# Performance work log

Measured on AMD Instinct MI355X. Metric: run time of the kernel, lower is better.

Reference implementation:

```python
import jax, jax.numpy as jnp
import numpy as np

NEG_SLOPE = 0.2  # PyG GATConv default


def _gat_layer(h_in, W, a_src, a_dst, b, src, dst, n_nodes, heads, out_dim):
    """One GATConv layer (PyG semantics: messages flow src -> dst,
    softmax over incoming edges of each dst node)."""
    h = (h_in @ W).reshape(n_nodes, heads, out_dim)          # [N,H,C]
    alpha_s = jnp.sum(h * a_src, axis=-1)                    # [N,H]
    alpha_d = jnp.sum(h * a_dst, axis=-1)                    # [N,H]
    e = jax.nn.leaky_relu(alpha_s[src] + alpha_d[dst], NEG_SLOPE)  # [E,H]
    # segment softmax over dst groups (numerically stable)
    m = jax.ops.segment_max(e, dst, num_segments=n_nodes)    # [N,H]
    ex = jnp.exp(e - m[dst])                                 # [E,H]
    s = jax.ops.segment_sum(ex, dst, num_segments=n_nodes)   # [N,H]
    alpha = ex / (s[dst] + 1e-16)                            # [E,H]
    msg = h[src] * alpha[:, :, None]                         # [E,H,C]
    out = jax.ops.segment_sum(msg, dst, num_segments=n_nodes)  # [N,H,C]
    return out.reshape(n_nodes, heads * out_dim) + b


def setup_inputs() -> dict:
    N, E = 50000, 800000
    IN, HID, H = 128, 64, 4
    key = jax.random.key(0)
    ks = jax.random.split(key, 10)
    x = jax.random.normal(ks[0], (N, IN), dtype=jnp.float32)
    edge_index = jax.random.randint(ks[1], (2, E), 0, N, dtype=jnp.int64)
    sc = 0.05
    return {
        "x": x,
        "edge_index": edge_index,
        "W1": jax.random.normal(ks[2], (IN, H * HID), dtype=jnp.float32) * sc,
        "att_src1": jax.random.normal(ks[3], (H, HID), dtype=jnp.float32) * sc,
        "att_dst1": jax.random.normal(ks[4], (H, HID), dtype=jnp.float32) * sc,
        "b1": jnp.zeros((H * HID,), dtype=jnp.float32),
        "W2": jax.random.normal(ks[5], (H * HID, HID), dtype=jnp.float32) * sc,
        "att_src2": jax.random.normal(ks[6], (1, HID), dtype=jnp.float32) * sc,
        "att_dst2": jax.random.normal(ks[7], (1, HID), dtype=jnp.float32) * sc,
        "b2": jnp.zeros((HID,), dtype=jnp.float32),
    }


def reference(x, edge_index, W1, att_src1, att_dst1, b1, W2, att_src2, att_dst2, b2):
    N = x.shape[0]
    H, HID = att_src1.shape
    # add self loops (PyG GATConv default add_self_loops=True)
    loops = jnp.arange(N, dtype=edge_index.dtype)
    src = jnp.concatenate([edge_index[0], loops])
    dst = jnp.concatenate([edge_index[1], loops])
    h = _gat_layer(x, W1, att_src1, att_dst1, b1, src, dst, N, H, HID)
    h = jax.nn.relu(h)
    out = _gat_layer(h, W2, att_src2, att_dst2, b2, src, dst, N, 1, HID)
    return out
```

## Files before the change

### kernel.cpp

```cpp
#include <hip/hip_runtime.h>
#include <cstdint>

#define LRELU_SLOPE 0.2f
#define ELL_K 48

typedef short bf16x8_t __attribute__((ext_vector_type(8)));
typedef float f32x4_t  __attribute__((ext_vector_type(4)));

__device__ __forceinline__ float bf2f(unsigned int u) { return __uint_as_float(u << 16); }
__device__ __forceinline__ unsigned short f2bf(float f) {
    unsigned int x = __float_as_uint(f);
    return (unsigned short)((x + 0x7fffu + ((x >> 16) & 1u)) >> 16);
}
__device__ __forceinline__ unsigned short f2h(float f) {
    union { unsigned short u; _Float16 h; } cv; cv.h = (_Float16)f; return cv.u;
}
__device__ __forceinline__ float h2f(unsigned short u) {
    union { unsigned short u; _Float16 h; } cv; cv.u = u; return (float)cv.h;
}

struct PrepDesc { const void* ssrc[6]; float* sdst[6]; int slen[6]; };
__global__ __launch_bounds__(256) void prep_k(const unsigned short* __restrict__ xh,
                                              const int* __restrict__ ei32,
                                              const void* __restrict__ w1raw,
                                              const void* __restrict__ w2raw,
                                              unsigned short* __restrict__ Wt1,
                                              unsigned short* __restrict__ Wt2,
                                              PrepDesc d, int* __restrict__ flags,
                                              int* __restrict__ deg, int N) {
    __shared__ int s_ei, s_cnt;
    if (threadIdx.x == 0) { s_ei = 0; s_cnt = 0; }
    __syncthreads();
    const int t = threadIdx.x;
    int e_or = 0;
#pragma unroll
    for (int j = 0; j < 4; j++) if (ei32[2 * (t * 4 + j) + 1] != 0) e_or = 1;
    if (e_or) atomicOr(&s_ei, 1);
    int c = 0;
#pragma unroll
    for (int j = 0; j < 8; j++) {
        unsigned short h = xh[t * 8 + j];
        int e = (h >> 7) & 0xFF;
        if (e >= 117 && e < 134) c++;
    }
    atomicAdd(&s_cnt, c);
    __syncthreads();
    const int isb = (s_cnt >= 1600) ? 1 : 0;
    if (blockIdx.x == 0 && t == 0) { flags[0] = s_ei; flags[1] = isb; }
    const int gstride = gridDim.x * blockDim.x;
    const int gid = blockIdx.x * blockDim.x + t;
    for (int i = gid; i < 128 * 256; i += gstride) {
        int k = i >> 8, n = i & 255;
        unsigned short b = isb ? ((const unsigned short*)w1raw)[i] : f2bf(((const float*)w1raw)[i]);
        Wt1[n * 128 + k] = b;
    }
    for (int i = gid; i < 256 * 64; i += gstride) {
        int k = i >> 6, n = i & 63;
        unsigned short b = isb ? ((const unsigned short*)w2raw)[i] : f2bf(((const float*)w2raw)[i]);
        Wt2[n * 256 + k] = b;
    }
#pragma unroll
    for (int s = 0; s < 6; s++)
        for (int i = gid; i < d.slen[s]; i += gstride) {
            float v = isb ? bf2f((unsigned int)((const unsigned short*)d.ssrc[s])[i])
                          : ((const float*)d.ssrc[s])[i];
            d.sdst[s][i] = v;
        }
    for (int i = gid; i < N; i += gstride) deg[i] = 0;
}

__global__ __launch_bounds__(256) void gemm1_k(const void* __restrict__ xraw,
                                               const unsigned short* __restrict__ Wt,
                                               const float* __restrict__ asw_,
                                               const float* __restrict__ adw_,
                                               unsigned short* __restrict__ h,
                                               float* __restrict__ as_, float* __restrict__ ad_,
                                               int M, const int* __restrict__ flags) {
    __shared__ unsigned short xs[64 * 136];
    const int tid = threadIdx.x;
    const long row0 = (long)blockIdx.x * 64;
    if (flags[1] != 0) {
        const uint4* xv = (const uint4*)xraw;
        const long base = row0 * 16;
        const long lim = (long)M * 16 - base;
#pragma unroll
        for (int i = 0; i < 4; i++) {
            int idx = tid + i * 256;
            uint4 v;
            if (idx < lim) v = xv[base + idx];
            else { v.x = v.y = v.z = v.w = 0u; }
            int r = idx >> 4, c8 = idx & 15;
            *(uint4*)&xs[r * 136 + c8 * 8] = v;
        }
    } else {
        const float4* xv = (const float4*)xraw;
        const long base = row0 * 32;
        const long lim = (long)M * 32 - base;
#pragma unroll
        for (int i = 0; i < 8; i++) {
            int idx = tid + i * 256;
            float4 v;
            if (idx < lim) v = xv[base + idx];
            else { v.x = v.y = v.z = v.w = 0.f; }
            int r = idx >> 5, c4 = idx & 31;
            ushort4 o;
            o.x = f2bf(v.x); o.y = f2bf(v.y); o.z = f2bf(v.z); o.w = f2bf(v.w);
            *(ushort4*)&xs[r * 136 + c4 * 4] = o;
        }
    }
    __syncthreads();
    const int wv = tid >> 6;
    const int lane = tid & 63;
    const int l16 = lane & 15, quad = lane >> 4;
    bf16x8_t af[4];
#pragma unroll
    for (int ks = 0; ks < 4; ks++)
        af[ks] = *(const bf16x8_t*)&xs[(wv * 16 + l16) * 136 + ks * 32 + quad * 8];
    float psA[4] = {0.f, 0.f, 0.f, 0.f}, pdA[4] = {0.f, 0.f, 0.f, 0.f};
#pragma unroll
    for (int t = 0; t < 16; t++) {
        f32x4_t acc = {0.f, 0.f, 0.f, 0.f};
#pragma unroll
        for (int ks = 0; ks < 4; ks++) {
            bf16x8_t bf = *(const bf16x8_t*)(Wt + (size_t)(t * 16 + l16) * 128 + ks * 32 + quad * 8);
            acc = __builtin_amdgcn_mfma_f32_16x16x32_bf16(af[ks], bf, acc, 0, 0, 0);
        }
        const float aswv = asw_[t * 16 + l16];
        const float adwv = adw_[t * 16 + l16];
#pragma unroll
        for (int r = 0; r < 4; r++) {
            long grow = row0 + wv * 16 + quad * 4 + r;
            if (grow < M) h[grow * 256 + t * 16 + l16] = f2bf(acc[r]);
            psA[r] = fmaf(acc[r], aswv, psA[r]);
            pdA[r] = fmaf(acc[r], adwv, pdA[r]);
        }
        if ((t & 3) == 3) {
            const int hd = t >> 2;
#pragma unroll
            for (int r = 0; r < 4; r++) {
                float ps = psA[r], pd = pdA[r];
#pragma unroll
                for (int o = 8; o > 0; o >>= 1) {
                    ps += __shfl_down(ps, o, 16);
                    pd += __shfl_down(pd, o, 16);
                }
                long grow = row0 + wv * 16 + quad * 4 + r;
                if (l16 == 0 && grow < M) { as_[grow * 4 + hd] = ps; ad_[grow * 4 + hd] = pd; }
                psA[r] = 0.f; pdA[r] = 0.f;
            }
        }
    }
}

__global__ void ell_k(const int* __restrict__ ei, int E, int N,
                      const int* __restrict__ flags, int* __restrict__ deg,
                      int* __restrict__ ell_src, uint2* __restrict__ ell_pw,
                      const float* __restrict__ as1, const float* __restrict__ ad1) {
    int i = blockIdx.x * blockDim.x + threadIdx.x;
    int T = E + N;
    if (i >= T) return;
    int is64 = (flags[0] == 0);
    int s, d;
    if (i < E) {
        s = is64 ? ei[2 * (long)i] : ei[i];
        long k = (long)E + i;
        d = is64 ? ei[2 * k] : ei[k];
    } else { s = d = i - E; }
    if ((unsigned)d >= (unsigned)N) return;
    if ((unsigned)s >= (unsigned)N) s = 0;
    int r = atomicAdd(&deg[d], 1);
    if (r >= ELL_K) return;
    long slot = (long)d * ELL_K + r;
    ell_src[slot] = s;
    float4 a = ((const float4*)as1)[s];
    float4 b = ((const float4*)ad1)[d];
    float e0 = a.x + b.x, e1 = a.y + b.y, e2 = a.z + b.z, e3 = a.w + b.w;
    e0 = e0 > 0.f ? e0 : LRELU_SLOPE * e0;
    e1 = e1 > 0.f ? e1 : LRELU_SLOPE * e1;
    e2 = e2 > 0.f ? e2 : LRELU_SLOPE * e2;
    e3 = e3 > 0.f ? e3 : LRELU_SLOPE * e3;
    uint2 p;
    p.x = (unsigned)f2h(__expf(e0)) | ((unsigned)f2h(__expf(e1)) << 16);
    p.y = (unsigned)f2h(__expf(e2)) | ((unsigned)f2h(__expf(e3)) << 16);
    ell_pw[slot] = p;
}

__global__ __launch_bounds__(256) void gemm2_k(const unsigned short* __restrict__ x,
                                               const unsigned short* __restrict__ Wt,
                                               const float* __restrict__ asw_,
                                               const float* __restrict__ adw_,
                                               unsigned short* __restrict__ h,
                                               float* __restrict__ as_, float* __restrict__ ad_,
                                               int M) {
    __shared__ unsigned short xs[64 * 264];
    const int tid = threadIdx.x;
    const long row0 = (long)blockIdx.x * 64;
    const uint4* xv = (const uint4*)x;
    const long base = row0 * 32;
    const long lim = (long)M * 32 - base;
#pragma unroll
    for (int i = 0; i < 8; i++) {
        int idx = tid + i * 256;
        uint4 v;
        if (idx < lim) v = xv[base + idx];
        else { v.x = v.y = v.z = v.w = 0u; }
        int r = idx >> 5, c8 = idx & 31;
        *(uint4*)&xs[r * 264 + c8 * 8] = v;
    }
    __syncthreads();
    const int wv = tid >> 6;
    const int lane = tid & 63;
    const int l16 = lane & 15, quad = lane >> 4;
    bf16x8_t af[8];
#pragma unroll
    for (int ks = 0; ks < 8; ks++)
        af[ks] = *(const bf16x8_t*)&xs[(wv * 16 + l16) * 264 + ks * 32 + quad * 8];
    float psA[4] = {0.f, 0.f, 0.f, 0.f}, pdA[4] = {0.f, 0.f, 0.f, 0.f};
#pragma unroll
    for (int t = 0; t < 4; t++) {
        f32x4_t acc = {0.f, 0.f, 0.f, 0.f};
#pragma unroll
        for (int ks = 0; ks < 8; ks++) {
            bf16x8_t bf = *(const bf16x8_t*)(Wt + (size_t)(t * 16 + l16) * 256 + ks * 32 + quad * 8);
            acc = __builtin_amdgcn_mfma_f32_16x16x32_bf16(af[ks], bf, acc, 0, 0, 0);
        }
        const float aswv = asw_[t * 16 + l16];
        const float adwv = adw_[t * 16 + l16];
#pragma unroll
        for (int r = 0; r < 4; r++) {
            long grow = row0 + wv * 16 + quad * 4 + r;
            if (grow < M) h[grow * 64 + t * 16 + l16] = f2bf(acc[r]);
            psA[r] = fmaf(acc[r], aswv, psA[r]);
            pdA[r] = fmaf(acc[r], adwv, pdA[r]);
        }
    }
#pragma unroll
    for (int r = 0; r < 4; r++) {
        float ps = psA[r], pd = pdA[r];
#pragma unroll
        for (int o = 8; o > 0; o >>= 1) { ps += __shfl_down(ps, o, 16); pd += __shfl_down(pd, o, 16); }
        long grow = row0 + wv * 16 + quad * 4 + r;
        if (l16 == 0 && grow < M) { as_[grow] = ps; ad_[grow] = pd; }
    }
}

#define B20(M) M(0) M(1) M(2) M(3) M(4) M(5) M(6) M(7) M(8) M(9) \
               M(10) M(11) M(12) M(13) M(14) M(15) M(16) M(17) M(18) M(19)

__global__ __launch_bounds__(256) void agg1_k(const uint4* __restrict__ hfeat,
                                              const int* __restrict__ deg,
                                              const int* __restrict__ ell_src,
                                              const uint2* __restrict__ ell_pw,
                                              const float* __restrict__ bias,
                                              unsigned short* __restrict__ outb, int N) {
    const int tid = threadIdx.x;
    const int g = tid >> 5;
    const int c = tid & 31;
    const long node = (long)blockIdx.x * 8 + g;
    if (node >= N) return;
    const int hh = c >> 3;
    const bool lo = hh < 2;
    const int sh = (hh & 1) << 4;
    const long beg = node * ELL_K;
    const int dv = deg[node];
    const int siA = ell_src[beg + c];
    const int siB = ell_src[beg + 32 + (c & 15)];
    const uint2 pAv = ell_pw[beg + c];
    const uint2 pBv = ell_pw[beg + 32 + (c & 15)];
    const unsigned pAx = pAv.x, pAy = pAv.y, pBx = pBv.x, pBy = pBv.y;
    const int cnt = dv < ELL_K ? dv : ELL_K;
    float a0 = 0.f, a1 = 0.f, a2 = 0.f, a3 = 0.f;
    float a4 = 0.f, a5 = 0.f, a6 = 0.f, a7 = 0.f, s = 0.f;
#define EDGE8(v, p) { \
        a0 = fmaf(p, __uint_as_float((v).x << 16), a0); \
        a1 = fmaf(p, __uint_as_float((v).x & 0xffff0000u), a1); \
        a2 = fmaf(p, __uint_as_float((v).y << 16), a2); \
        a3 = fmaf(p, __uint_as_float((v).y & 0xffff0000u), a3); \
        a4 = fmaf(p, __uint_as_float((v).z << 16), a4); \
        a5 = fmaf(p, __uint_as_float((v).z & 0xffff0000u), a5); \
        a6 = fmaf(p, __uint_as_float((v).w << 16), a6); \
        a7 = fmaf(p, __uint_as_float((v).w & 0xffff0000u), a7); \
        s += p; }
#define DECL1(k) uint4 vv##k;
#define ISSUE1(k) if (j + k < cnt) { \
        const int e = j + k; \
        const int sv = __shfl((e < 32) ? siA : siB, e & 31, 32); \
        vv##k = hfeat[(long)sv * 32 + c]; }
#define CONS1(k) if (j + k < cnt) { \
        const int e = j + k; \
        const unsigned bx = (unsigned)__shfl((int)((e < 32) ? pAx : pBx), e & 31, 32); \
        const unsigned by = (unsigned)__shfl((int)((e < 32) ? pAy : pBy), e & 31, 32); \
        const unsigned pwu = lo ? bx : by; \
        const float p = h2f((unsigned short)((pwu >> sh) & 0xffffu)); \
        EDGE8(vv##k, p) }
    {
        const int j = 0;
        B20(DECL1)
        B20(ISSUE1)
        B20(CONS1)
    }
    if (cnt > 20) {
        const int j = 20;
        B20(DECL1)
        B20(ISSUE1)
        B20(CONS1)
        if (cnt > 40) {
            const int j2 = 40;
#define ISSUE1b(k) if (j2 + k < cnt) { \
            const int e = j2 + k; \
            const int sv = __shfl((e < 32) ? siA : siB, e & 31, 32); \
            vv##k = hfeat[(long)sv * 32 + c]; }
#define CONS1b(k) if (j2 + k < cnt) { \
            const int e = j2 + k; \
            const unsigned bx = (unsigned)__shfl((int)((e < 32) ? pAx : pBx), e & 31, 32); \
            const unsigned by = (unsigned)__shfl((int)((e < 32) ? pAy : pBy), e & 31, 32); \
            const unsigned pwu = lo ? bx : by; \
            const float p = h2f((unsigned short)((pwu >> sh) & 0xffffu)); \
            EDGE8(vv##k, p) }
            ISSUE1b(0) ISSUE1b(1) ISSUE1b(2) ISSUE1b(3)
            ISSUE1b(4) ISSUE1b(5) ISSUE1b(6) ISSUE1b(7)
            CONS1b(0) CONS1b(1) CONS1b(2) CONS1b(3)
            CONS1b(4) CONS1b(5) CONS1b(6) CONS1b(7)
#undef ISSUE1b
#undef CONS1b
        }
    }
#undef DECL1
#undef ISSUE1
#undef CONS1
#undef EDGE8
    const float4 b0 = ((const float4*)bias)[2 * c];
    const float4 b1 = ((const float4*)bias)[2 * c + 1];
    const float inv = 1.f / s;
    uint4 o;
    o.x = (unsigned)f2bf(fmaxf(fmaf(a0, inv, b0.x), 0.f)) |
          ((unsigned)f2bf(fmaxf(fmaf(a1, inv, b0.y), 0.f)) << 16);
    o.y = (unsigned)f2bf(fmaxf(fmaf(a2, inv, b0.z), 0.f)) |
          ((unsigned)f2bf(fmaxf(fmaf(a3, inv, b0.w), 0.f)) << 16);
    o.z = (unsigned)f2bf(fmaxf(fmaf(a4, inv, b1.x), 0.f)) |
          ((unsigned)f2bf(fmaxf(fmaf(a5, inv, b1.y), 0.f)) << 16);
    o.w = (unsigned)f2bf(fmaxf(fmaf(a6, inv, b1.z), 0.f)) |
          ((unsigned)f2bf(fmaxf(fmaf(a7, inv, b1.w), 0.f)) << 16);
    ((uint4*)outb)[node * 32 + c] = o;
}

__global__ __launch_bounds__(256) void agg2_k(const unsigned short* __restrict__ hfeat,
                                              const float* __restrict__ as_,
                                              const float* __restrict__ ad_,
                                              const int* __restrict__ deg,
                                              const int* __restrict__ ell_src,
                                              const float* __restrict__ bias,
                                              unsigned short* __restrict__ outb,
                                              float* __restrict__ outf,
                                              const int* __restrict__ flags, int N) {
    const int tid = threadIdx.x;
    const int g = tid >> 4;
    const int c = tid & 15;
    const long node = (long)blockIdx.x * 16 + g;
    if (node >= N) return;
    const long beg = node * ELL_K;
    const int dv = deg[node];
    const int rA = ell_src[beg + c];
    const int rB = ell_src[beg + 16 + c];
    const int rC = ell_src[beg + 32 + c];
    const float adn = ad_[node];
    const int cnt = dv < ELL_K ? dv : ELL_K;
    const int sA = (c      < cnt) ? rA : 0;
    const int sB = (c + 16 < cnt) ? rB : 0;
    const int sC = (c + 32 < cnt) ? rC : 0;
    const float avA = as_[sA];
    const float avB = as_[sB];
    const float avC = as_[sC];
    const uint2* hv = (const uint2*)hfeat;
    float sm = 0.f, a0 = 0.f, a1 = 0.f, a2 = 0.f, a3 = 0.f;
#define EDGE4(v, p) { \
        a0 = fmaf(p, __uint_as_float((v).x << 16), a0); \
        a1 = fmaf(p, __uint_as_float((v).x & 0xffff0000u), a1); \
        a2 = fmaf(p, __uint_as_float((v).y << 16), a2); \
        a3 = fmaf(p, __uint_as_float((v).y & 0xffff0000u), a3); \
        sm += p; }
#define DECL2(k) uint2 vv##k;
#define ISSUE2(k) if (j + k < cnt) { \
        const int e = j + k; \
        const int sv = __shfl((e < 16) ? sA : ((e < 32) ? sB : sC), e & 15, 16); \
        vv##k = hv[(long)sv * 16 + c]; }
#define CONS2(k) if (j + k < cnt) { \
        const int e = j + k; \
        const float av = __shfl((e < 16) ? avA : ((e < 32) ? avB : avC), e & 15, 16); \
        float t = av + adn; t = t > 0.f ? t : LRELU_SLOPE * t; \
        const float p = __expf(t); \
        EDGE4(vv##k, p) }
    {
        const int j = 0;
        B20(DECL2)
        B20(ISSUE2)
        B20(CONS2)
    }
    if (cnt > 20) {
        const int j = 20;
        B20(DECL2)
        B20(ISSUE2)
        B20(CONS2)
        if (cnt > 40) {
            const int j2 = 40;
#define ISSUE2b(k) if (j2 + k < cnt) { \
            const int e = j2 + k; \
            const int sv = __shfl((e < 16) ? sA : ((e < 32) ? sB : sC), e & 15, 16); \
            vv##k = hv[(long)sv * 16 + c]; }
#define CONS2b(k) if (j2 + k < cnt) { \
            const int e = j2 + k; \
            const float av = __shfl((e < 16) ? avA : ((e < 32) ? avB : avC), e & 15, 16); \
            float t = av + adn; t = t > 0.f ? t : LRELU_SLOPE * t; \
            const float p = __expf(t); \
            EDGE4(vv##k, p) }
            ISSUE2b(0) ISSUE2b(1) ISSUE2b(2) ISSUE2b(3)
            ISSUE2b(4) ISSUE2b(5) ISSUE2b(6) ISSUE2b(7)
            CONS2b(0) CONS2b(1) CONS2b(2) CONS2b(3)
            CONS2b(4) CONS2b(5) CONS2b(6) CONS2b(7)
#undef ISSUE2b
#undef CONS2b
        }
    }
#undef DECL2
#undef ISSUE2
#undef CONS2
#undef EDGE4
    const float inv = 1.f / sm;
    const float4 bi = ((const float4*)bias)[c];
    const float v0 = fmaf(a0, inv, bi.x);
    const float v1 = fmaf(a1, inv, bi.y);
    const float v2 = fmaf(a2, inv, bi.z);
    const float v3 = fmaf(a3, inv, bi.w);
    if (flags[1] != 0) {
        uint2 o;
        o.x = (unsigned)f2bf(v0) | ((unsigned)f2bf(v1) << 16);
        o.y = (unsigned)f2bf(v2) | ((unsigned)f2bf(v3) << 16);
        ((uint2*)outb)[node * 16 + c] = o;
    } else {
        float4 o; o.x = v0; o.y = v1; o.z = v2; o.w = v3;
        ((float4*)outf)[node * 16 + c] = o;
    }
}

static inline size_t alignup(size_t v, size_t a) { return (v + a - 1) & ~(a - 1); }

extern "C" void kernel_launch(void* const* d_in, const int* in_sizes, int n_in,
                              void* d_out, int out_size, void* d_ws, size_t ws_size,
                              hipStream_t stream) {
    const void* x  = d_in[0];
    const int*  ei = (const int*)d_in[1];

    const int N = in_sizes[0] / 128;
    const int E = in_sizes[1] / 2;
    const int T = E + N;

    size_t off = 0;
    char* w = (char*)d_ws;
    auto take = [&](size_t bytes) { void* p = w + off; off = alignup(off + bytes, 256); return p; };

    int*   flags = (int*)take(256);
    unsigned short* Wt1 = (unsigned short*)take((size_t)256 * 128 * 2);
    unsigned short* Wt2 = (unsigned short*)take((size_t)64 * 256 * 2);
    float* as1w = (float*)take(256 * 4);
    float* ad1w = (float*)take(256 * 4);
    float* b1f  = (float*)take(256 * 4);
    float* as2w = (float*)take(64 * 4);
    float* ad2w = (float*)take(64 * 4);
    float* b2f  = (float*)take(64 * 4);
    unsigned short* h1b   = (unsigned short*)take((size_t)N * 256 * 2);
    unsigned short* act1b = (unsigned short*)take((size_t)N * 256 * 2);
    float* as1 = (float*)take((size_t)N * 4 * 4);
    float* ad1 = (float*)take((size_t)N * 4 * 4);
    float* as2 = (float*)take((size_t)N * 4);
    float* ad2 = (float*)take((size_t)N * 4);
    int* deg   = (int*)take((size_t)N * 4);
    int* ell_src = (int*)take((size_t)N * ELL_K * 4);
    uint2* ell_pw = (uint2*)take((size_t)N * ELL_K * 8);
    unsigned short* h2b = h1b;

    PrepDesc pd;
    pd.ssrc[0] = d_in[3]; pd.sdst[0] = as1w; pd.slen[0] = 256;
    pd.ssrc[1] = d_in[4]; pd.sdst[1] = ad1w; pd.slen[1] = 256;
    pd.ssrc[2] = d_in[5]; pd.sdst[2] = b1f;  pd.slen[2] = 256;
    pd.ssrc[3] = d_in[7]; pd.sdst[3] = as2w; pd.slen[3] = 64;
    pd.ssrc[4] = d_in[8]; pd.sdst[4] = ad2w; pd.slen[4] = 64;
    pd.ssrc[5] = d_in[9]; pd.sdst[5] = b2f;  pd.slen[5] = 64;
    prep_k<<<64, 256, 0, stream>>>((const unsigned short*)x, ei, d_in[2], d_in[6],
                                   Wt1, Wt2, pd, flags, deg, N);

    gemm1_k<<<(N + 63) / 64, 256, 0, stream>>>(x, Wt1, as1w, ad1w, h1b, as1, ad1, N, flags);
    ell_k<<<(T + 255) / 256, 256, 0, stream>>>(ei, E, N, flags, deg, ell_src, ell_pw, as1, ad1);
    agg1_k<<<(N + 7) / 8, 256, 0, stream>>>((const uint4*)h1b, deg, ell_src, ell_pw, b1f, act1b, N);
    gemm2_k<<<(N + 63) / 64, 256, 0, stream>>>(act1b, Wt2, as2w, ad2w, h2b, as2, ad2, N);
    agg2_k<<<(N + 15) / 16, 256, 0, stream>>>(h2b, as2, ad2, deg, ell_src, b2f,
                                              (unsigned short*)d_out, (float*)d_out, flags, N);
}
```

Baseline: 290.2 us.

## Fuse layer-2 GEMM into layer-1 aggregation kernel via LDS tile

The layer-1 aggregation now writes its 8 activated node rows into shared memory, and one wave then runs the layer-2 MFMA projection plus the attention dot products in the same block. This drops the separate gemm2 launch and the write and reread of the N×256 bf16 activation buffer. In exchange, each block pads its 16-row MFMA tile with 8 zero rows, so half the MFMA work is wasted. It also adds a __syncthreads and a serial GEMM tail on one wave while the other three sit idle, and every block rereads Wt2 from cache.

```diff
diff --git a/kernel.cpp b/kernel.cpp
--- a/kernel.cpp
+++ b/kernel.cpp
@@ -185,90 +185,45 @@
     ell_pw[slot] = p;
 }
 
-__global__ __launch_bounds__(256) void gemm2_k(const unsigned short* __restrict__ x,
-                                               const unsigned short* __restrict__ Wt,
-                                               const float* __restrict__ asw_,
-                                               const float* __restrict__ adw_,
-                                               unsigned short* __restrict__ h,
-                                               float* __restrict__ as_, float* __restrict__ ad_,
-                                               int M) {
-    __shared__ unsigned short xs[64 * 264];
-    const int tid = threadIdx.x;
-    const long row0 = (long)blockIdx.x * 64;
-    const uint4* xv = (const uint4*)x;
-    const long base = row0 * 32;
-    const long lim = (long)M * 32 - base;
-#pragma unroll
-    for (int i = 0; i < 8; i++) {
-        int idx = tid + i * 256;
-        uint4 v;
-        if (idx < lim) v = xv[base + idx];
-        else { v.x = v.y = v.z = v.w = 0u; }
-        int r = idx >> 5, c8 = idx & 31;
-        *(uint4*)&xs[r * 264 + c8 * 8] = v;
-    }
-    __syncthreads();
-    const int wv = tid >> 6;
-    const int lane = tid & 63;
-    const int l16 = lane & 15, quad = lane >> 4;
-    bf16x8_t af[8];
-#pragma unroll
-    for (int ks = 0; ks < 8; ks++)
-        af[ks] = *(const bf16x8_t*)&xs[(wv * 16 + l16) * 264 + ks * 32 + quad * 8];
-    float psA[4] = {0.f, 0.f, 0.f, 0.f}, pdA[4] = {0.f, 0.f, 0.f, 0.f};
-#pragma unroll
-    for (int t = 0; t < 4; t++) {
-        f32x4_t acc = {0.f, 0.f, 0.f, 0.f};
-#pragma unroll
-        for (int ks = 0; ks < 8; ks++) {
-            bf16x8_t bf = *(const bf16x8_t*)(Wt + (size_t)(t * 16 + l16) * 256 + ks * 32 + quad * 8);
-            acc = __builtin_amdgcn_mfma_f32_16x16x32_bf16(af[ks], bf, acc, 0, 0, 0);
-        }
-        const float aswv = asw_[t * 16 + l16];
-        const float adwv = adw_[t * 16 + l16];
-#pragma unroll
-        for (int r = 0; r < 4; r++) {
-            long grow = row0 + wv * 16 + quad * 4 + r;
-            if (grow < M) h[grow * 64 + t * 16 + l16] = f2bf(acc[r]);
-            psA[r] = fmaf(acc[r], aswv, psA[r]);
-            pdA[r] = fmaf(acc[r], adwv, pdA[r]);
-        }
-    }
-#pragma unroll
-    for (int r = 0; r < 4; r++) {
-        float ps = psA[r], pd = pdA[r];
-#pragma unroll
-        for (int o = 8; o > 0; o >>= 1) { ps += __shfl_down(ps, o, 16); pd += __shfl_down(pd, o, 16); }
-        long grow = row0 + wv * 16 + quad * 4 + r;
-        if (l16 == 0 && grow < M) { as_[grow] = ps; ad_[grow] = pd; }
-    }
-}
-
 #define B20(M) M(0) M(1) M(2) M(3) M(4) M(5) M(6) M(7) M(8) M(9) \
                M(10) M(11) M(12) M(13) M(14) M(15) M(16) M(17) M(18) M(19)
 
-__global__ __launch_bounds__(256) void agg1_k(const uint4* __restrict__ hfeat,
-                                              const int* __restrict__ deg,
-                                              const int* __restrict__ ell_src,
-                                              const uint2* __restrict__ ell_pw,
-                                              const float* __restrict__ bias,
-                                              unsigned short* __restrict__ outb, int N) {
+__global__ __launch_bounds__(256) void agg1g2_k(const uint4* __restrict__ hfeat,
+                                                const int* __restrict__ deg,
+                                                const int* __restrict__ ell_src,
+                                                const uint2* __restrict__ ell_pw,
+                                                const float* __restrict__ bias,
+                                                const unsigned short* __restrict__ Wt2,
+                                                const float* __restrict__ asw2,
+                                                const float* __restrict__ adw2,
+                                                unsigned short* __restrict__ h2,
+                                                float* __restrict__ as2,
+                                                float* __restrict__ ad2, int N) {
+    __shared__ unsigned short act_lds[16 * 264];
     const int tid = threadIdx.x;
     const int g = tid >> 5;
     const int c = tid & 31;
     const long node = (long)blockIdx.x * 8 + g;
-    if (node >= N) return;
+    const bool valid = node < N;
+    {
+        uint4 z; z.x = z.y = z.z = z.w = 0u;
+        for (int i = tid; i < 264; i += 256) ((uint4*)(act_lds + 8 * 264))[i] = z;
+    }
     const int hh = c >> 3;
     const bool lo = hh < 2;
     const int sh = (hh & 1) << 4;
     const long beg = node * ELL_K;
-    const int dv = deg[node];
-    const int siA = ell_src[beg + c];
-    const int siB = ell_src[beg + 32 + (c & 15)];
-    const uint2 pAv = ell_pw[beg + c];
-    const uint2 pBv = ell_pw[beg + 32 + (c & 15)];
-    const unsigned pAx = pAv.x, pAy = pAv.y, pBx = pBv.x, pBy = pBv.y;
-    const int cnt = dv < ELL_K ? dv : ELL_K;
+    int dv = 0, siA = 0, siB = 0;
+    unsigned pAx = 0, pAy = 0, pBx = 0, pBy = 0;
+    if (valid) {
+        dv = deg[node];
+        siA = ell_src[beg + c];
+        siB = ell_src[beg + 32 + (c & 15)];
+        const uint2 pAv = ell_pw[beg + c];
+        const uint2 pBv = ell_pw[beg + 32 + (c & 15)];
+        pAx = pAv.x; pAy = pAv.y; pBx = pBv.x; pBy = pBv.y;
+    }
+    const int cnt = valid ? (dv < ELL_K ? dv : ELL_K) : 0;
     float a0 = 0.f, a1 = 0.f, a2 = 0.f, a3 = 0.f;
     float a4 = 0.f, a5 = 0.f, a6 = 0.f, a7 = 0.f, s = 0.f;
 #define EDGE8(v, p) { \
@@ -331,7 +286,7 @@
 #undef EDGE8
     const float4 b0 = ((const float4*)bias)[2 * c];
     const float4 b1 = ((const float4*)bias)[2 * c + 1];
-    const float inv = 1.f / s;
+    const float inv = (s > 0.f) ? 1.f / s : 0.f;
     uint4 o;
     o.x = (unsigned)f2bf(fmaxf(fmaf(a0, inv, b0.x), 0.f)) |
           ((unsigned)f2bf(fmaxf(fmaf(a1, inv, b0.y), 0.f)) << 16);
@@ -341,7 +296,47 @@
           ((unsigned)f2bf(fmaxf(fmaf(a5, inv, b1.y), 0.f)) << 16);
     o.w = (unsigned)f2bf(fmaxf(fmaf(a6, inv, b1.z), 0.f)) |
           ((unsigned)f2bf(fmaxf(fmaf(a7, inv, b1.w), 0.f)) << 16);
-    ((uint4*)outb)[node * 32 + c] = o;
+    *(uint4*)&act_lds[g * 264 + c * 8] = o;
+    __syncthreads();
+    if (tid < 64) {
+        const int l16 = tid & 15, quad = tid >> 4;
+        bf16x8_t af[8];
+#pragma unroll
+        for (int ks = 0; ks < 8; ks++)
+            af[ks] = *(const bf16x8_t*)&act_lds[l16 * 264 + ks * 32 + quad * 8];
+        float psA[4] = {0.f, 0.f, 0.f, 0.f}, pdA[4] = {0.f, 0.f, 0.f, 0.f};
+#pragma unroll
+        for (int t = 0; t < 4; t++) {
+            f32x4_t acc = {0.f, 0.f, 0.f, 0.f};
+#pragma unroll
+            for (int ks = 0; ks < 8; ks++) {
+                bf16x8_t bf = *(const bf16x8_t*)(Wt2 + (size_t)(t * 16 + l16) * 256 + ks * 32 + quad * 8);
+                acc = __builtin_amdgcn_mfma_f32_16x16x32_bf16(af[ks], bf, acc, 0, 0, 0);
+            }
+            const float aswv = asw2[t * 16 + l16];
+            const float adwv = adw2[t * 16 + l16];
+#pragma unroll
+            for (int r = 0; r < 4; r++) {
+                const int row8 = quad * 4 + r;
+                const long gn = (long)blockIdx.x * 8 + row8;
+                if (row8 < 8 && gn < N) h2[gn * 64 + t * 16 + l16] = f2bf(acc[r]);
+                psA[r] = fmaf(acc[r], aswv, psA[r]);
+                pdA[r] = fmaf(acc[r], adwv, pdA[r]);
+            }
+        }
+#pragma unroll
+        for (int r = 0; r < 4; r++) {
+            float ps = psA[r], pd = pdA[r];
+#pragma unroll
+            for (int o2 = 8; o2 > 0; o2 >>= 1) {
+                ps += __shfl_down(ps, o2, 16);
+                pd += __shfl_down(pd, o2, 16);
+            }
+            const int row8 = quad * 4 + r;
+            const long gn = (long)blockIdx.x * 8 + row8;
+            if (l16 == 0 && row8 < 8 && gn < N) { as2[gn] = ps; ad2[gn] = pd; }
+        }
+    }
 }
 
 __global__ __launch_bounds__(256) void agg2_k(const unsigned short* __restrict__ hfeat,
@@ -467,8 +462,8 @@
     float* as2w = (float*)take(64 * 4);
     float* ad2w = (float*)take(64 * 4);
     float* b2f  = (float*)take(64 * 4);
-    unsigned short* h1b   = (unsigned short*)take((size_t)N * 256 * 2);
-    unsigned short* act1b = (unsigned short*)take((size_t)N * 256 * 2);
+    unsigned short* h1b = (unsigned short*)take((size_t)N * 256 * 2);
+    unsigned short* h2b = (unsigned short*)take((size_t)N * 64 * 2);
     float* as1 = (float*)take((size_t)N * 4 * 4);
     float* ad1 = (float*)take((size_t)N * 4 * 4);
     float* as2 = (float*)take((size_t)N * 4);
@@ -476,7 +471,6 @@
     int* deg   = (int*)take((size_t)N * 4);
     int* ell_src = (int*)take((size_t)N * ELL_K * 4);
     uint2* ell_pw = (uint2*)take((size_t)N * ELL_K * 8);
-    unsigned short* h2b = h1b;
 
     PrepDesc pd;
     pd.ssrc[0] = d_in[3]; pd.sdst[0] = as1w; pd.slen[0] = 256;
@@ -490,8 +484,8 @@
 
     gemm1_k<<<(N + 63) / 64, 256, 0, stream>>>(x, Wt1, as1w, ad1w, h1b, as1, ad1, N, flags);
     ell_k<<<(T + 255) / 256, 256, 0, stream>>>(ei, E, N, flags, deg, ell_src, ell_pw, as1, ad1);
-    agg1_k<<<(N + 7) / 8, 256, 0, stream>>>((const uint4*)h1b, deg, ell_src, ell_pw, b1f, act1b, N);
-    gemm2_k<<<(N + 63) / 64, 256, 0, stream>>>(act1b, Wt2, as2w, ad2w, h2b, as2, ad2, N);
+    agg1g2_k<<<(N + 7) / 8, 256, 0, stream>>>((const uint4*)h1b, deg, ell_src, ell_pw, b1f,
+                                              Wt2, as2w, ad2w, h2b, as2, ad2, N);
     agg2_k<<<(N + 15) / 16, 256, 0, stream>>>(h2b, as2, ad2, deg, ell_src, b2f,
                                               (unsigned short*)d_out, (float*)d_out, flags, N);
 }
```

Result: faster. 273.9 us (-5.6%).
